# Kernel tuning notes

Hardware: AMD Instinct MI355X
Metric: run time of the kernel (lower is better)

## Reference

```python
import jax, jax.numpy as jnp
import numpy as np

T, B = 4096, 8192


def setup_inputs() -> dict:
    key = jax.random.key(0)
    k1, k2 = jax.random.split(key)
    # binary Bernoulli(0.5) observations, shape [T, B, 1]
    inputs = jnp.round(jax.random.uniform(k1, (T, B, 1), dtype=jnp.float32))
    # decay_rate = exp(-1 / 10**loglifetime), loglifetime ~ U(0.5, 2.5)
    loglifetime = jax.random.uniform(k2, (), minval=0.5, maxval=2.5)
    decay_rate = jnp.exp(-1.0 / (10.0 ** loglifetime)).astype(jnp.float32)
    return {"inputs": inputs, "decay_rate": decay_rate}


def _forward(inputs, decay_rate):
    # order == 1 ('transition' estimate): bigram leaky counts
    x = inputs[:, :, 0]                      # [T, B]
    n_seqs = x.shape[1]
    z = jnp.zeros((n_seqs,), dtype=inputs.dtype)
    d = decay_rate

    def step(carry, x_t):
        n10, n11, na0, na1, prev = carry
        n10 = d * (n10 + x_t * (1.0 - prev))   # ones after a 0
        n11 = d * (n11 + x_t * prev)           # ones after a 1
        na0 = d * (na0 + (1.0 - prev))         # all after a 0
        na1 = d * (na1 + prev)                 # all after a 1
        return (n10, n11, na0, na1, x_t), (n10, n11, na0, na1)

    _, (n10s, n11s, na0s, na1s) = jax.lax.scan(step, (z, z, z, z, z), x)

    N_ONES_PRIOR, N_ALL_PRIOR = 1.0, 2.0
    p0 = (n10s + N_ONES_PRIOR) / (na0s + N_ALL_PRIOR)   # [T, B]
    p1 = (n11s + N_ONES_PRIOR) / (na1s + N_ALL_PRIOR)   # [T, B]
    # prediction conditioned on current observation
    pred = p0 * (1.0 - x) + p1 * x                      # [T, B]
    return pred[:, :, None]                             # [T, B, 1]


def reference(inputs, decay_rate):
    return _forward(inputs, decay_rate)
```

## Files before the change

kernel.cpp:

```cpp
#include <hip/hip_runtime.h>


constexpr int T_DIM  = 4096;
constexpr int B_DIM  = 8192;
constexpr int NCHUNK = 64;
constexpr int CLEN   = T_DIM / NCHUNK;
constexpr int VEC    = 4;
constexpr int UNROLL = 8;

typedef float v4f __attribute__((ext_vector_type(4)));
typedef unsigned long long u64;
typedef u64 v2u __attribute__((ext_vector_type(2)));

__global__ __launch_bounds__(256) void partial_kernel(
    const float* __restrict__ x, const float* __restrict__ dptr,
    float* __restrict__ ws)
{
    const float d  = *dptr;
    const int   c  = blockIdx.y;
    const int   b0 = (blockIdx.x * blockDim.x + threadIdx.x) * VEC;
    const long  t0 = (long)c * CLEN;

    float prev[VEC];
    if (c == 0) {
        #pragma unroll
        for (int j = 0; j < VEC; ++j) prev[j] = 0.0f;
    } else {
        const v4f pv = *reinterpret_cast<const v4f*>(x + (t0 - 1) * B_DIM + b0);
        #pragma unroll
        for (int j = 0; j < VEC; ++j) prev[j] = pv[j];
    }

    float m[VEC]   = {0.f, 0.f, 0.f, 0.f};
    float n11[VEC] = {0.f, 0.f, 0.f, 0.f};
    u64   mask[VEC] = {0ull, 0ull, 0ull, 0ull};

    const float* p = x + t0 * B_DIM + b0;

    v4f A[UNROLL], Bv[UNROLL];
    #pragma unroll
    for (int u = 0; u < UNROLL; ++u)
        A[u] = *reinterpret_cast<const v4f*>(p + (size_t)u * B_DIM);

    auto compute = [&](const v4f* buf, int kbase) {
        #pragma unroll
        for (int u = 0; u < UNROLL; ++u) {
            const int k = kbase + u;
            #pragma unroll
            for (int j = 0; j < VEC; ++j) {
                const float xt = buf[u][j];
                mask[j] |= (u64)(unsigned)xt << k;
                m[j]   = d * (m[j] + xt);
                n11[j] = d * (n11[j] + xt * prev[j]);
                prev[j] = xt;
            }
        }
    };

    #pragma unroll
    for (int kk = 0; kk < CLEN; kk += 2 * UNROLL) {
        #pragma unroll
        for (int u = 0; u < UNROLL; ++u)
            Bv[u] = *reinterpret_cast<const v4f*>(p + (size_t)(kk + UNROLL + u) * B_DIM);
        compute(A, kk);
        if (kk + 2 * UNROLL < CLEN) {
            #pragma unroll
            for (int u = 0; u < UNROLL; ++u)
                A[u] = *reinterpret_cast<const v4f*>(p + (size_t)(kk + 2 * UNROLL + u) * B_DIM);
        }
        compute(Bv, kk + UNROLL);
    }

    float* wm = ws + (size_t)c * B_DIM + b0;
    v4f mv, nv;
    #pragma unroll
    for (int j = 0; j < VEC; ++j) { mv[j] = m[j]; nv[j] = n11[j]; }
    *reinterpret_cast<v4f*>(wm)                                = mv;
    *reinterpret_cast<v4f*>(wm + (size_t)NCHUNK * B_DIM)       = nv;

    u64* bits = reinterpret_cast<u64*>(ws + (size_t)2 * NCHUNK * B_DIM);
    v2u b01, b23;
    b01[0] = mask[0]; b01[1] = mask[1];
    b23[0] = mask[2]; b23[1] = mask[3];
    *reinterpret_cast<v2u*>(&bits[(size_t)c * B_DIM + b0])     = b01;
    *reinterpret_cast<v2u*>(&bits[(size_t)c * B_DIM + b0 + 2]) = b23;
}

__global__ __launch_bounds__(256) void scan_kernel(
    const float* __restrict__ dptr, float* __restrict__ ws)
{
    float dL = *dptr;
    #pragma unroll
    for (int i = 0; i < 6; ++i) dL = dL * dL;

    const int tid = blockIdx.x * blockDim.x + threadIdx.x;
    float* p = ws + (size_t)(tid >> 13) * NCHUNK * B_DIM + (tid & (B_DIM - 1));

    float l[NCHUNK];
    #pragma unroll
    for (int c = 0; c < NCHUNK; ++c) l[c] = p[(size_t)c * B_DIM];

    float s = 0.f;
    #pragma unroll
    for (int c = 0; c < NCHUNK; ++c) {
        p[(size_t)c * B_DIM] = s;
        s = dL * s + l[c];
    }
}

__global__ __launch_bounds__(256) void final_kernel(
    const float* __restrict__ dptr, const float* __restrict__ ws,
    float* __restrict__ out)
{
    const float d = *dptr;
    float dL = d;
    #pragma unroll
    for (int i = 0; i < 6; ++i) dL = dL * dL;

    const int c  = blockIdx.y;
    const int b0 = (blockIdx.x * blockDim.x + threadIdx.x) * VEC;

    const float* w = ws + (size_t)c * B_DIM + b0;
    const v4f mi = *reinterpret_cast<const v4f*>(w);
    const v4f ni = *reinterpret_cast<const v4f*>(w + (size_t)NCHUNK * B_DIM);
    float m[VEC], n11[VEC];
    #pragma unroll
    for (int j = 0; j < VEC; ++j) { m[j] = mi[j]; n11[j] = ni[j]; }

    float dLc = 1.f, sq = dL;
    int cc = c;
    #pragma unroll
    for (int i = 0; i < 6; ++i) { if (cc & 1) dLc *= sq; sq *= sq; cc >>= 1; }
    float na = d * (1.f - dLc) / (1.f - d);

    const u64* bits = reinterpret_cast<const u64*>(ws + (size_t)2 * NCHUNK * B_DIM);
    u64 mask[VEC];
    #pragma unroll
    for (int j = 0; j < VEC; ++j) mask[j] = bits[(size_t)c * B_DIM + b0 + j];

    bool pb[VEC];
    if (c == 0) {
        #pragma unroll
        for (int j = 0; j < VEC; ++j) pb[j] = false;
    } else {
        #pragma unroll
        for (int j = 0; j < VEC; ++j)
            pb[j] = (bits[(size_t)(c - 1) * B_DIM + b0 + j] >> 63) & 1ull;
    }

    float* q = out + (size_t)c * CLEN * B_DIM + b0;
    for (int kk = 0; kk < CLEN; kk += UNROLL) {
        #pragma unroll
        for (int u = 0; u < UNROLL; ++u) {
            const int k = kk + u;
            na = d * (na + 1.f);
            float pr[VEC];
            #pragma unroll
            for (int j = 0; j < VEC; ++j) {
                const bool  xb = (mask[j] >> k) & 1ull;
                const float mo = m[j];
                m[j]   = d * (mo + (xb ? 1.f : 0.f));
                n11[j] = d * (n11[j] + ((xb && pb[j]) ? 1.f : 0.f));
                const float num = xb ? (n11[j] + 1.f) : (m[j] - n11[j] + 1.f);
                const float den = xb ? (mo + 2.f)     : (na - mo + 2.f);
                pr[j] = num * __builtin_amdgcn_rcpf(den);
                pb[j] = xb;
            }
            v4f ov;
            #pragma unroll
            for (int j = 0; j < VEC; ++j) ov[j] = pr[j];
            __builtin_nontemporal_store(ov, reinterpret_cast<v4f*>(q + (size_t)u * B_DIM));
        }
        q += (size_t)UNROLL * B_DIM;
    }
}

extern "C" void kernel_launch(void* const* d_in, const int* in_sizes, int n_in,
                              void* d_out, int out_size, void* d_ws, size_t ws_size,
                              hipStream_t stream) {
    const float* x  = (const float*)d_in[0];
    const float* dr = (const float*)d_in[1];
    float* ws  = (float*)d_ws;
    float* out = (float*)d_out;

    dim3 blk(256);
    dim3 grid1(B_DIM / VEC / 256, NCHUNK);
    partial_kernel<<<grid1, blk, 0, stream>>>(x, dr, ws);
    scan_kernel<<<(2 * B_DIM) / 256, blk, 0, stream>>>(dr, ws);
    final_kernel<<<grid1, blk, 0, stream>>>(dr, ws, out);
}
```

Measured before the change: 239.2 us.

## Fuse partial, scan and final kernels into one with inter-block flag synchronization

Merges the three-kernel chunked scan into a single kernel. Each block publishes its chunk partials, sets a release flag, then waits on the flags of all earlier chunks and sums their decayed partials itself. The bit masks and the previous observation stay in registers, so the mask workspace round trip and two launches go away. In exchange it adds a memset, spin-waiting that relies on earlier chunks being scheduled first (grid is only 8x64 blocks, so all should be resident), and an O(c) redundant prefix computation per block.

```diff
diff --git a/kernel.cpp b/kernel.cpp
--- a/kernel.cpp
+++ b/kernel.cpp
@@ -7,36 +7,44 @@
 constexpr int CLEN   = T_DIM / NCHUNK;
 constexpr int VEC    = 4;
 constexpr int UNROLL = 8;
+constexpr int BLOCK  = 256;
+constexpr int NSLAB  = B_DIM / (BLOCK * VEC);
 
 typedef float v4f __attribute__((ext_vector_type(4)));
 typedef unsigned long long u64;
-typedef u64 v2u __attribute__((ext_vector_type(2)));
 
-__global__ __launch_bounds__(256) void partial_kernel(
+__global__ __launch_bounds__(BLOCK) void fused_kernel(
     const float* __restrict__ x, const float* __restrict__ dptr,
-    float* __restrict__ ws)
+    float* __restrict__ ws, float* __restrict__ out)
 {
-    const float d  = *dptr;
-    const int   c  = blockIdx.y;
-    const int   b0 = (blockIdx.x * blockDim.x + threadIdx.x) * VEC;
-    const long  t0 = (long)c * CLEN;
+    const float d = *dptr;
+    float dL = d;
+    #pragma unroll
+    for (int i = 0; i < 6; ++i) dL = dL * dL;
 
-    float prev[VEC];
+    const int  c  = blockIdx.y;
+    const int  s  = blockIdx.x;
+    const int  b0 = s * (BLOCK * VEC) + (int)threadIdx.x * VEC;
+    const long t0 = (long)c * CLEN;
+
+    float pinit[VEC];
     if (c == 0) {
         #pragma unroll
-        for (int j = 0; j < VEC; ++j) prev[j] = 0.0f;
+        for (int j = 0; j < VEC; ++j) pinit[j] = 0.0f;
     } else {
         const v4f pv = *reinterpret_cast<const v4f*>(x + (t0 - 1) * B_DIM + b0);
         #pragma unroll
-        for (int j = 0; j < VEC; ++j) prev[j] = pv[j];
+        for (int j = 0; j < VEC; ++j) pinit[j] = pv[j];
     }
 
     float m[VEC]   = {0.f, 0.f, 0.f, 0.f};
     float n11[VEC] = {0.f, 0.f, 0.f, 0.f};
     u64   mask[VEC] = {0ull, 0ull, 0ull, 0ull};
+    float prev[VEC];
+    #pragma unroll
+    for (int j = 0; j < VEC; ++j) prev[j] = pinit[j];
 
     const float* p = x + t0 * B_DIM + b0;
-
     v4f A[UNROLL], Bv[UNROLL];
     #pragma unroll
     for (int u = 0; u < UNROLL; ++u)
@@ -71,61 +79,63 @@
         compute(Bv, kk + UNROLL);
     }
 
-    float* wm = ws + (size_t)c * B_DIM + b0;
-    v4f mv, nv;
-    #pragma unroll
-    for (int j = 0; j < VEC; ++j) { mv[j] = m[j]; nv[j] = n11[j]; }
-    *reinterpret_cast<v4f*>(wm)                                = mv;
-    *reinterpret_cast<v4f*>(wm + (size_t)NCHUNK * B_DIM)       = nv;
+    {
+        float* wm = ws + (size_t)c * B_DIM + b0;
+        v4f mv, nv;
+        #pragma unroll
+        for (int j = 0; j < VEC; ++j) { mv[j] = m[j]; nv[j] = n11[j]; }
+        *reinterpret_cast<v4f*>(wm)                          = mv;
+        *reinterpret_cast<v4f*>(wm + (size_t)NCHUNK * B_DIM) = nv;
+    }
+    __threadfence();
+    __syncthreads();
+    int* flags = reinterpret_cast<int*>(ws + (size_t)2 * NCHUNK * B_DIM);
+    if (threadIdx.x == 0)
+        __hip_atomic_store(&flags[c * NSLAB + s], 1,
+                           __ATOMIC_RELEASE, __HIP_MEMORY_SCOPE_AGENT);
 
-    u64* bits = reinterpret_cast<u64*>(ws + (size_t)2 * NCHUNK * B_DIM);
-    v2u b01, b23;
-    b01[0] = mask[0]; b01[1] = mask[1];
-    b23[0] = mask[2]; b23[1] = mask[3];
-    *reinterpret_cast<v2u*>(&bits[(size_t)c * B_DIM + b0])     = b01;
-    *reinterpret_cast<v2u*>(&bits[(size_t)c * B_DIM + b0 + 2]) = b23;
-}
+    float sm[VEC] = {0.f, 0.f, 0.f, 0.f};
+    float sn[VEC] = {0.f, 0.f, 0.f, 0.f};
+    if (c > 0) {
+        if ((int)threadIdx.x < c) {
+            const int* f = &flags[(int)threadIdx.x * NSLAB + s];
+            while (__hip_atomic_load(f, __ATOMIC_RELAXED,
+                                     __HIP_MEMORY_SCOPE_AGENT) == 0)
+                __builtin_amdgcn_s_sleep(8);
+        }
+        __syncthreads();
+        __threadfence();
 
-__global__ __launch_bounds__(256) void scan_kernel(
-    const float* __restrict__ dptr, float* __restrict__ ws)
-{
-    float dL = *dptr;
-    #pragma unroll
-    for (int i = 0; i < 6; ++i) dL = dL * dL;
-
-    const int tid = blockIdx.x * blockDim.x + threadIdx.x;
-    float* p = ws + (size_t)(tid >> 13) * NCHUNK * B_DIM + (tid & (B_DIM - 1));
-
-    float l[NCHUNK];
-    #pragma unroll
-    for (int c = 0; c < NCHUNK; ++c) l[c] = p[(size_t)c * B_DIM];
-
-    float s = 0.f;
-    #pragma unroll
-    for (int c = 0; c < NCHUNK; ++c) {
-        p[(size_t)c * B_DIM] = s;
-        s = dL * s + l[c];
+        const float* lm = ws + b0;
+        const float* ln = ws + (size_t)NCHUNK * B_DIM + b0;
+        int cp = 0;
+        for (; cp + 4 <= c; cp += 4) {
+            v4f a0 = *reinterpret_cast<const v4f*>(lm + (size_t)(cp + 0) * B_DIM);
+            v4f a1 = *reinterpret_cast<const v4f*>(lm + (size_t)(cp + 1) * B_DIM);
+            v4f a2 = *reinterpret_cast<const v4f*>(lm + (size_t)(cp + 2) * B_DIM);
+            v4f a3 = *reinterpret_cast<const v4f*>(lm + (size_t)(cp + 3) * B_DIM);
+            v4f e0 = *reinterpret_cast<const v4f*>(ln + (size_t)(cp + 0) * B_DIM);
+            v4f e1 = *reinterpret_cast<const v4f*>(ln + (size_t)(cp + 1) * B_DIM);
+            v4f e2 = *reinterpret_cast<const v4f*>(ln + (size_t)(cp + 2) * B_DIM);
+            v4f e3 = *reinterpret_cast<const v4f*>(ln + (size_t)(cp + 3) * B_DIM);
+            #pragma unroll
+            for (int j = 0; j < VEC; ++j) {
+                sm[j] = dL * sm[j] + a0[j];  sn[j] = dL * sn[j] + e0[j];
+                sm[j] = dL * sm[j] + a1[j];  sn[j] = dL * sn[j] + e1[j];
+                sm[j] = dL * sm[j] + a2[j];  sn[j] = dL * sn[j] + e2[j];
+                sm[j] = dL * sm[j] + a3[j];  sn[j] = dL * sn[j] + e3[j];
+            }
+        }
+        for (; cp < c; ++cp) {
+            v4f a = *reinterpret_cast<const v4f*>(lm + (size_t)cp * B_DIM);
+            v4f e = *reinterpret_cast<const v4f*>(ln + (size_t)cp * B_DIM);
+            #pragma unroll
+            for (int j = 0; j < VEC; ++j) {
+                sm[j] = dL * sm[j] + a[j];
+                sn[j] = dL * sn[j] + e[j];
+            }
+        }
     }
-}
-
-__global__ __launch_bounds__(256) void final_kernel(
-    const float* __restrict__ dptr, const float* __restrict__ ws,
-    float* __restrict__ out)
-{
-    const float d = *dptr;
-    float dL = d;
-    #pragma unroll
-    for (int i = 0; i < 6; ++i) dL = dL * dL;
-
-    const int c  = blockIdx.y;
-    const int b0 = (blockIdx.x * blockDim.x + threadIdx.x) * VEC;
-
-    const float* w = ws + (size_t)c * B_DIM + b0;
-    const v4f mi = *reinterpret_cast<const v4f*>(w);
-    const v4f ni = *reinterpret_cast<const v4f*>(w + (size_t)NCHUNK * B_DIM);
-    float m[VEC], n11[VEC];
-    #pragma unroll
-    for (int j = 0; j < VEC; ++j) { m[j] = mi[j]; n11[j] = ni[j]; }
 
     float dLc = 1.f, sq = dL;
     int cc = c;
@@ -133,19 +143,11 @@
     for (int i = 0; i < 6; ++i) { if (cc & 1) dLc *= sq; sq *= sq; cc >>= 1; }
     float na = d * (1.f - dLc) / (1.f - d);
 
-    const u64* bits = reinterpret_cast<const u64*>(ws + (size_t)2 * NCHUNK * B_DIM);
-    u64 mask[VEC];
+    float M[VEC], N11[VEC];
+    bool  pb[VEC];
     #pragma unroll
-    for (int j = 0; j < VEC; ++j) mask[j] = bits[(size_t)c * B_DIM + b0 + j];
-
-    bool pb[VEC];
-    if (c == 0) {
-        #pragma unroll
-        for (int j = 0; j < VEC; ++j) pb[j] = false;
-    } else {
-        #pragma unroll
-        for (int j = 0; j < VEC; ++j)
-            pb[j] = (bits[(size_t)(c - 1) * B_DIM + b0 + j] >> 63) & 1ull;
+    for (int j = 0; j < VEC; ++j) {
+        M[j] = sm[j]; N11[j] = sn[j]; pb[j] = (pinit[j] != 0.0f);
     }
 
     float* q = out + (size_t)c * CLEN * B_DIM + b0;
@@ -158,10 +160,10 @@
             #pragma unroll
             for (int j = 0; j < VEC; ++j) {
                 const bool  xb = (mask[j] >> k) & 1ull;
-                const float mo = m[j];
-                m[j]   = d * (mo + (xb ? 1.f : 0.f));
-                n11[j] = d * (n11[j] + ((xb && pb[j]) ? 1.f : 0.f));
-                const float num = xb ? (n11[j] + 1.f) : (m[j] - n11[j] + 1.f);
+                const float mo = M[j];
+                M[j]   = d * (mo + (xb ? 1.f : 0.f));
+                N11[j] = d * (N11[j] + ((xb && pb[j]) ? 1.f : 0.f));
+                const float num = xb ? (N11[j] + 1.f) : (M[j] - N11[j] + 1.f);
                 const float den = xb ? (mo + 2.f)     : (na - mo + 2.f);
                 pr[j] = num * __builtin_amdgcn_rcpf(den);
                 pb[j] = xb;
@@ -183,9 +185,10 @@
     float* ws  = (float*)d_ws;
     float* out = (float*)d_out;
 
-    dim3 blk(256);
-    dim3 grid1(B_DIM / VEC / 256, NCHUNK);
-    partial_kernel<<<grid1, blk, 0, stream>>>(x, dr, ws);
-    scan_kernel<<<(2 * B_DIM) / 256, blk, 0, stream>>>(dr, ws);
-    final_kernel<<<grid1, blk, 0, stream>>>(dr, ws, out);
+    void* flags = (void*)((char*)d_ws + (size_t)2 * NCHUNK * B_DIM * sizeof(float));
+    hipMemsetAsync(flags, 0, NCHUNK * NSLAB * sizeof(int), stream);
+
+    dim3 blk(BLOCK);
+    dim3 grid(NSLAB, NCHUNK);
+    fused_kernel<<<grid, blk, 0, stream>>>(x, dr, ws, out);
 }
```

Measured after the change: 358.9 us. 1.5x slower.

## Double chunk count, shrink bitmasks to 32-bit, and pipeline the chunk scan

Applied to the files above, without the earlier changes.

Splits the time axis into 128 chunks of 32 steps instead of 64 chunks of 64 steps. This doubles the number of blocks in the partial and final passes, and each observation bitmask now fits in 32 bits, so masks are loaded and stored as one vector. The carry scan now runs in 64-thread blocks and loads its 128 chunk values in two double-buffered groups of 32. Workspace writes become nontemporal, and launch bounds add an occupancy hint. The cost is a longer sequential scan over twice as many chunk carries and more workspace traffic.

```diff
diff --git a/kernel.cpp b/kernel.cpp
--- a/kernel.cpp
+++ b/kernel.cpp
@@ -3,22 +3,23 @@
 
 constexpr int T_DIM  = 4096;
 constexpr int B_DIM  = 8192;
-constexpr int NCHUNK = 64;
+constexpr int NCHUNK = 128;
 constexpr int CLEN   = T_DIM / NCHUNK;
 constexpr int VEC    = 4;
-constexpr int UNROLL = 8;
+constexpr int UNROLL = 4;
+constexpr int BLOCK  = 256;
 
 typedef float v4f __attribute__((ext_vector_type(4)));
-typedef unsigned long long u64;
-typedef u64 v2u __attribute__((ext_vector_type(2)));
-
-__global__ __launch_bounds__(256) void partial_kernel(
+typedef unsigned int u32;
+typedef u32 v4u __attribute__((ext_vector_type(4)));
+
+__global__ __launch_bounds__(BLOCK, 4) void partial_kernel(
     const float* __restrict__ x, const float* __restrict__ dptr,
     float* __restrict__ ws)
 {
     const float d  = *dptr;
     const int   c  = blockIdx.y;
-    const int   b0 = (blockIdx.x * blockDim.x + threadIdx.x) * VEC;
+    const int   b0 = (blockIdx.x * BLOCK + (int)threadIdx.x) * VEC;
     const long  t0 = (long)c * CLEN;
 
     float prev[VEC];
@@ -33,7 +34,7 @@
 
     float m[VEC]   = {0.f, 0.f, 0.f, 0.f};
     float n11[VEC] = {0.f, 0.f, 0.f, 0.f};
-    u64   mask[VEC] = {0ull, 0ull, 0ull, 0ull};
+    u32   mask[VEC] = {0u, 0u, 0u, 0u};
 
     const float* p = x + t0 * B_DIM + b0;
 
@@ -49,7 +50,7 @@
             #pragma unroll
             for (int j = 0; j < VEC; ++j) {
                 const float xt = buf[u][j];
-                mask[j] |= (u64)(unsigned)xt << k;
+                mask[j] |= (u32)xt << k;
                 m[j]   = d * (m[j] + xt);
                 n11[j] = d * (n11[j] + xt * prev[j]);
                 prev[j] = xt;
@@ -75,50 +76,63 @@
     v4f mv, nv;
     #pragma unroll
     for (int j = 0; j < VEC; ++j) { mv[j] = m[j]; nv[j] = n11[j]; }
-    *reinterpret_cast<v4f*>(wm)                                = mv;
-    *reinterpret_cast<v4f*>(wm + (size_t)NCHUNK * B_DIM)       = nv;
-
-    u64* bits = reinterpret_cast<u64*>(ws + (size_t)2 * NCHUNK * B_DIM);
-    v2u b01, b23;
-    b01[0] = mask[0]; b01[1] = mask[1];
-    b23[0] = mask[2]; b23[1] = mask[3];
-    *reinterpret_cast<v2u*>(&bits[(size_t)c * B_DIM + b0])     = b01;
-    *reinterpret_cast<v2u*>(&bits[(size_t)c * B_DIM + b0 + 2]) = b23;
-}
-
-__global__ __launch_bounds__(256) void scan_kernel(
+    __builtin_nontemporal_store(mv, reinterpret_cast<v4f*>(wm));
+    __builtin_nontemporal_store(nv, reinterpret_cast<v4f*>(wm + (size_t)NCHUNK * B_DIM));
+
+    u32* bits = reinterpret_cast<u32*>(ws + (size_t)2 * NCHUNK * B_DIM);
+    v4u bm;
+    #pragma unroll
+    for (int j = 0; j < VEC; ++j) bm[j] = mask[j];
+    __builtin_nontemporal_store(bm, reinterpret_cast<v4u*>(&bits[(size_t)c * B_DIM + b0]));
+}
+
+__global__ __launch_bounds__(64) void scan_kernel(
     const float* __restrict__ dptr, float* __restrict__ ws)
 {
     float dL = *dptr;
     #pragma unroll
-    for (int i = 0; i < 6; ++i) dL = dL * dL;
-
-    const int tid = blockIdx.x * blockDim.x + threadIdx.x;
+    for (int i = 0; i < 5; ++i) dL = dL * dL;
+
+    const int tid = blockIdx.x * 64 + (int)threadIdx.x;
     float* p = ws + (size_t)(tid >> 13) * NCHUNK * B_DIM + (tid & (B_DIM - 1));
 
-    float l[NCHUNK];
-    #pragma unroll
-    for (int c = 0; c < NCHUNK; ++c) l[c] = p[(size_t)c * B_DIM];
+    constexpr int G  = 32;
+    constexpr int NG = NCHUNK / G;
+    float cur[G], nxt[G];
+    #pragma unroll
+    for (int i = 0; i < G; ++i) cur[i] = p[(size_t)i * B_DIM];
 
     float s = 0.f;
     #pragma unroll
-    for (int c = 0; c < NCHUNK; ++c) {
-        p[(size_t)c * B_DIM] = s;
-        s = dL * s + l[c];
-    }
-}
-
-__global__ __launch_bounds__(256) void final_kernel(
+    for (int g = 0; g < NG; ++g) {
+        if (g + 1 < NG) {
+            #pragma unroll
+            for (int i = 0; i < G; ++i)
+                nxt[i] = p[(size_t)((g + 1) * G + i) * B_DIM];
+        }
+        #pragma unroll
+        for (int i = 0; i < G; ++i) {
+            p[(size_t)(g * G + i) * B_DIM] = s;
+            s = dL * s + cur[i];
+        }
+        if (g + 1 < NG) {
+            #pragma unroll
+            for (int i = 0; i < G; ++i) cur[i] = nxt[i];
+        }
+    }
+}
+
+__global__ __launch_bounds__(BLOCK, 4) void final_kernel(
     const float* __restrict__ dptr, const float* __restrict__ ws,
     float* __restrict__ out)
 {
     const float d = *dptr;
     float dL = d;
     #pragma unroll
-    for (int i = 0; i < 6; ++i) dL = dL * dL;
+    for (int i = 0; i < 5; ++i) dL = dL * dL;
 
     const int c  = blockIdx.y;
-    const int b0 = (blockIdx.x * blockDim.x + threadIdx.x) * VEC;
+    const int b0 = (blockIdx.x * BLOCK + (int)threadIdx.x) * VEC;
 
     const float* w = ws + (size_t)c * B_DIM + b0;
     const v4f mi = *reinterpret_cast<const v4f*>(w);
@@ -130,25 +144,27 @@
     float dLc = 1.f, sq = dL;
     int cc = c;
     #pragma unroll
-    for (int i = 0; i < 6; ++i) { if (cc & 1) dLc *= sq; sq *= sq; cc >>= 1; }
+    for (int i = 0; i < 7; ++i) { if (cc & 1) dLc *= sq; sq *= sq; cc >>= 1; }
     float na = d * (1.f - dLc) / (1.f - d);
 
-    const u64* bits = reinterpret_cast<const u64*>(ws + (size_t)2 * NCHUNK * B_DIM);
-    u64 mask[VEC];
-    #pragma unroll
-    for (int j = 0; j < VEC; ++j) mask[j] = bits[(size_t)c * B_DIM + b0 + j];
+    const u32* bits = reinterpret_cast<const u32*>(ws + (size_t)2 * NCHUNK * B_DIM);
+    const v4u bm = *reinterpret_cast<const v4u*>(&bits[(size_t)c * B_DIM + b0]);
+    u32 mask[VEC];
+    #pragma unroll
+    for (int j = 0; j < VEC; ++j) mask[j] = bm[j];
 
     bool pb[VEC];
     if (c == 0) {
         #pragma unroll
         for (int j = 0; j < VEC; ++j) pb[j] = false;
     } else {
-        #pragma unroll
-        for (int j = 0; j < VEC; ++j)
-            pb[j] = (bits[(size_t)(c - 1) * B_DIM + b0 + j] >> 63) & 1ull;
+        const v4u pm = *reinterpret_cast<const v4u*>(&bits[(size_t)(c - 1) * B_DIM + b0]);
+        #pragma unroll
+        for (int j = 0; j < VEC; ++j) pb[j] = (pm[j] >> 31) & 1u;
     }
 
     float* q = out + (size_t)c * CLEN * B_DIM + b0;
+    #pragma unroll
     for (int kk = 0; kk < CLEN; kk += UNROLL) {
         #pragma unroll
         for (int u = 0; u < UNROLL; ++u) {
@@ -157,7 +173,7 @@
             float pr[VEC];
             #pragma unroll
             for (int j = 0; j < VEC; ++j) {
-                const bool  xb = (mask[j] >> k) & 1ull;
+                const bool  xb = (mask[j] >> k) & 1u;
                 const float mo = m[j];
                 m[j]   = d * (mo + (xb ? 1.f : 0.f));
                 n11[j] = d * (n11[j] + ((xb && pb[j]) ? 1.f : 0.f));
@@ -183,9 +199,9 @@
     float* ws  = (float*)d_ws;
     float* out = (float*)d_out;
 
-    dim3 blk(256);
-    dim3 grid1(B_DIM / VEC / 256, NCHUNK);
+    dim3 blk(BLOCK);
+    dim3 grid1(B_DIM / VEC / BLOCK, NCHUNK);
     partial_kernel<<<grid1, blk, 0, stream>>>(x, dr, ws);
-    scan_kernel<<<(2 * B_DIM) / 256, blk, 0, stream>>>(dr, ws);
+    scan_kernel<<<(2 * B_DIM) / 64, dim3(64), 0, stream>>>(dr, ws);
     final_kernel<<<grid1, blk, 0, stream>>>(dr, ws, out);
 }
```

Result: no change. 243.2 us (+1.6%).
